# Performance work log

Measured on AMD Instinct MI355X. Metric: run time of the kernel, lower is better.

## Reference

```python
import jax, jax.numpy as jnp
import numpy as np

HIDDEN = 1024
HEADS = 16
HEAD_DIM = HIDDEN // HEADS
LN_EPS = 1e-12
NEG = -1.0e9


def setup_inputs() -> dict:
    key = jax.random.key(0)
    ks = jax.random.split(key, 12)
    B, S = 2, 2048
    sc = 1.0 / np.sqrt(HIDDEN)
    inp = {
        "x": jax.random.normal(ks[0], (B, S, HIDDEN), dtype=jnp.float32),
        "attention_mask": jax.random.randint(ks[1], (B, S, S), 0, 2, dtype=jnp.int32),
        "Wq": jax.random.normal(ks[2], (HIDDEN, HIDDEN), dtype=jnp.float32) * sc,
        "bq": jnp.zeros((HIDDEN,), dtype=jnp.float32),
        "Wk": jax.random.normal(ks[3], (HIDDEN, HIDDEN), dtype=jnp.float32) * sc,
        "bk": jnp.zeros((HIDDEN,), dtype=jnp.float32),
        "Wv": jax.random.normal(ks[4], (HIDDEN, HIDDEN), dtype=jnp.float32) * sc,
        "bv": jnp.zeros((HIDDEN,), dtype=jnp.float32),
        "Wo": jax.random.normal(ks[5], (HIDDEN, HIDDEN), dtype=jnp.float32) * sc,
        "bo": jnp.zeros((HIDDEN,), dtype=jnp.float32),
        "ln_g": jnp.ones((HIDDEN,), dtype=jnp.float32),
        "ln_b": jnp.zeros((HIDDEN,), dtype=jnp.float32),
    }
    return inp


def _heads(t):  # [B,S,HIDDEN] -> [B,H,S,D]
    B, S, _ = t.shape
    return t.reshape(B, S, HEADS, HEAD_DIM).transpose(0, 2, 1, 3)


def reference(x, attention_mask, Wq, bq, Wk, bk, Wv, bv, Wo, bo, ln_g, ln_b):
    q = _heads(x @ Wq + bq)
    k = _heads(x @ Wk + bk)
    v = _heads(x @ Wv + bv)
    # [B,H,Sq,Sk]
    scores = jnp.einsum("bhqd,bhkd->bhqk", q, k) / np.sqrt(HEAD_DIM).astype(np.float32)
    mask = attention_mask[:, None, :, :] == 0
    scores = jnp.where(mask, NEG, scores)
    probs = jax.nn.softmax(scores, axis=-1)
    ctx = jnp.einsum("bhqk,bhkd->bhqd", probs, v)
    B, _, S, _ = ctx.shape
    ctx = ctx.transpose(0, 2, 1, 3).reshape(B, S, HIDDEN)
    h = ctx @ Wo + bo
    y = h + x
    mu = jnp.mean(y, axis=-1, keepdims=True)
    var = jnp.mean(jnp.square(y - mu), axis=-1, keepdims=True)
    out = (y - mu) * jax.lax.rsqrt(var + LN_EPS) * ln_g + ln_b
    return out, scores
```

## Files before the change

kernel.cpp:

```cpp
#include <hip/hip_runtime.h>
#include <math.h>

#define HIDDEN 1024
#define HEADS 16
#define HDIM 64
#define BATCH 2
#define SEQ 2048
#define NEGV -1.0e9f
#define TOK (BATCH * SEQ * HIDDEN)
#define SC_N ((size_t)BATCH * HEADS * SEQ * SEQ)
#define ROW_CUT 29
#define PIT 72

typedef __bf16 bf16x8 __attribute__((ext_vector_type(8)));
typedef float f32x4 __attribute__((ext_vector_type(4)));

__device__ __forceinline__ unsigned short f2bf(float f) {
    union { float f; unsigned u; } v; v.f = f;
    unsigned r = (v.u + 0x7fffu + ((v.u >> 16) & 1u)) >> 16;
    return (unsigned short)r;
}
__device__ __forceinline__ float bf2f(unsigned short h) {
    union { unsigned u; float f; } v; v.u = ((unsigned)h) << 16;
    return v.f;
}
__device__ __forceinline__ void split_bf(float v, unsigned short& h, unsigned short& l) {
    h = f2bf(v);
    l = f2bf(v - bf2f(h));
}
__device__ __forceinline__ bf16x8 ld_frag(const unsigned short* p) {
    union { uint4 u; bf16x8 v; } t;
    t.u = *(const uint4*)p;
    return t.v;
}

template<int PRESPLIT, int SPLITOUT>
__global__ __launch_bounds__(256) void mfma_gemm(
    const float* __restrict__ A,
    const unsigned short* __restrict__ Ahi, const unsigned short* __restrict__ Alo,
    const float* __restrict__ Bw, const float* __restrict__ bias,
    float* __restrict__ C,
    unsigned short* __restrict__ Ohi, unsigned short* __restrict__ Olo,
    int M, int N, int K)
{
    __shared__ unsigned short Ah[128][PIT], Al[128][PIT];
    __shared__ unsigned short Bh[64][PIT], Bl[64][PIT];
    int tid = threadIdx.x;
    int lane = tid & 63, wv = tid >> 6;
    int wm = wv >> 1, wn = wv & 1;
    int l15 = lane & 15, l4 = lane >> 4;
    int mBase = blockIdx.y * 128, nBase = blockIdx.x * 64;

    f32x4 acc[4][2] = {};

    for (int kt = 0; kt < K; kt += 64) {
        if (PRESPLIT) {
            int r = tid >> 3, g = tid & 7;
            #pragma unroll
            for (int i = 0; i < 4; i++) {
                int rr = r + i * 32;
                size_t gofs = (size_t)(mBase + rr) * K + kt + g * 8;
                *(uint4*)&Ah[rr][g * 8] = *(const uint4*)&Ahi[gofs];
                *(uint4*)&Al[rr][g * 8] = *(const uint4*)&Alo[gofs];
            }
        } else {
            int r = tid >> 4, c4 = (tid & 15) * 4;
            #pragma unroll
            for (int i = 0; i < 8; i++) {
                int rr = r + i * 16;
                float4 f = *(const float4*)&A[(size_t)(mBase + rr) * K + kt + c4];
                unsigned short h0, h1, h2, h3, q0, q1, q2, q3;
                split_bf(f.x, h0, q0); split_bf(f.y, h1, q1);
                split_bf(f.z, h2, q2); split_bf(f.w, h3, q3);
                uint2 ph, pl;
                ph.x = (unsigned)h0 | ((unsigned)h1 << 16);
                ph.y = (unsigned)h2 | ((unsigned)h3 << 16);
                pl.x = (unsigned)q0 | ((unsigned)q1 << 16);
                pl.y = (unsigned)q2 | ((unsigned)q3 << 16);
                *(uint2*)&Ah[rr][c4] = ph;
                *(uint2*)&Al[rr][c4] = pl;
            }
        }
        {
            int r = tid >> 4, c4 = (tid & 15) * 4;
            #pragma unroll
            for (int i = 0; i < 4; i++) {
                int rr = r + i * 16;
                float4 f = *(const float4*)&Bw[(size_t)(kt + rr) * N + nBase + c4];
                unsigned short h, l;
                split_bf(f.x, h, l); Bh[c4 + 0][rr] = h; Bl[c4 + 0][rr] = l;
                split_bf(f.y, h, l); Bh[c4 + 1][rr] = h; Bl[c4 + 1][rr] = l;
                split_bf(f.z, h, l); Bh[c4 + 2][rr] = h; Bl[c4 + 2][rr] = l;
                split_bf(f.w, h, l); Bh[c4 + 3][rr] = h; Bl[c4 + 3][rr] = l;
            }
        }
        __syncthreads();

        #pragma unroll
        for (int ks = 0; ks < 64; ks += 32) {
            int ko = ks + l4 * 8;
            bf16x8 aH[4], aL[4], bH[2], bL[2];
            #pragma unroll
            for (int ti = 0; ti < 4; ti++) {
                aH[ti] = ld_frag(&Ah[wm * 64 + ti * 16 + l15][ko]);
                aL[ti] = ld_frag(&Al[wm * 64 + ti * 16 + l15][ko]);
            }
            #pragma unroll
            for (int tj = 0; tj < 2; tj++) {
                bH[tj] = ld_frag(&Bh[wn * 32 + tj * 16 + l15][ko]);
                bL[tj] = ld_frag(&Bl[wn * 32 + tj * 16 + l15][ko]);
            }
            #pragma unroll
            for (int ti = 0; ti < 4; ti++)
                #pragma unroll
                for (int tj = 0; tj < 2; tj++) {
                    acc[ti][tj] = __builtin_amdgcn_mfma_f32_16x16x32_bf16(aH[ti], bH[tj], acc[ti][tj], 0, 0, 0);
                    acc[ti][tj] = __builtin_amdgcn_mfma_f32_16x16x32_bf16(aH[ti], bL[tj], acc[ti][tj], 0, 0, 0);
                    acc[ti][tj] = __builtin_amdgcn_mfma_f32_16x16x32_bf16(aL[ti], bH[tj], acc[ti][tj], 0, 0, 0);
                }
        }
        __syncthreads();
    }

    #pragma unroll
    for (int ti = 0; ti < 4; ti++) {
        #pragma unroll
        for (int tj = 0; tj < 2; tj++) {
            int m0 = mBase + wm * 64 + ti * 16 + l4 * 4;
            int n  = nBase + wn * 32 + tj * 16 + l15;
            float bv = bias[n];
            #pragma unroll
            for (int rg = 0; rg < 4; rg++) {
                float v = acc[ti][tj][rg] + bv;
                if (SPLITOUT) {
                    unsigned short h, l;
                    split_bf(v, h, l);
                    Ohi[(size_t)(m0 + rg) * N + n] = h;
                    Olo[(size_t)(m0 + rg) * N + n] = l;
                } else {
                    C[(size_t)(m0 + rg) * N + n] = v;
                }
            }
        }
    }
}

__global__ __launch_bounds__(256) void attn_mfma(
    const unsigned short* __restrict__ Qhi, const unsigned short* __restrict__ Qlo,
    const unsigned short* __restrict__ Khi, const unsigned short* __restrict__ Klo,
    const unsigned short* __restrict__ Vhi, const unsigned short* __restrict__ Vlo,
    const int* __restrict__ mask, float* __restrict__ scores_out,
    unsigned short* __restrict__ Chi, unsigned short* __restrict__ Clo)
{
    __shared__ unsigned short Kh[64][PIT], Kl[64][PIT];
    __shared__ unsigned short Th[64][PIT], Tl[64][PIT];
    __shared__ unsigned short Ph[4][16][PIT], Pl[4][16][PIT];

    int tid = threadIdx.x;
    int lane = tid & 63, w = tid >> 6;
    int l15 = lane & 15, l4 = lane >> 4;
    int qBase = blockIdx.x * 64;
    int h = blockIdx.y, b = blockIdx.z;

    size_t qofs = (size_t)(b * SEQ + qBase + w * 16 + l15) * HIDDEN + h * HDIM;
    bf16x8 qh0 = ld_frag(&Qhi[qofs + l4 * 8]);
    bf16x8 qh1 = ld_frag(&Qhi[qofs + 32 + l4 * 8]);
    bf16x8 ql0 = ld_frag(&Qlo[qofs + l4 * 8]);
    bf16x8 ql1 = ld_frag(&Qlo[qofs + 32 + l4 * 8]);

    f32x4 cacc[4] = {};
    float mrow[4] = {-3.0e38f, -3.0e38f, -3.0e38f, -3.0e38f};
    float rsum[4] = {0.f, 0.f, 0.f, 0.f};

    for (int kt = 0; kt < SEQ; kt += 64) {
        {
            int r = tid >> 3, g = tid & 7;
            #pragma unroll
            for (int i = 0; i < 2; i++) {
                int rr = r + i * 32;
                size_t tok = (size_t)(b * SEQ + kt + rr) * HIDDEN + h * HDIM + g * 8;
                *(uint4*)&Kh[rr][g * 8] = *(const uint4*)&Khi[tok];
                *(uint4*)&Kl[rr][g * 8] = *(const uint4*)&Klo[tok];
                union { uint4 u; unsigned short s[8]; } vh, vl;
                vh.u = *(const uint4*)&Vhi[tok];
                vl.u = *(const uint4*)&Vlo[tok];
                #pragma unroll
                for (int dd = 0; dd < 8; dd++) {
                    Th[g * 8 + dd][rr] = vh.s[dd];
                    Tl[g * 8 + dd][rr] = vl.s[dd];
                }
            }
        }
        __syncthreads();

        f32x4 sacc[4] = {};
        #pragma unroll
        for (int ks = 0; ks < 64; ks += 32) {
            int ko = ks + l4 * 8;
            bf16x8 qH = ks ? qh1 : qh0;
            bf16x8 qL = ks ? ql1 : ql0;
            #pragma unroll
            for (int j = 0; j < 4; j++) {
                bf16x8 kH = ld_frag(&Kh[j * 16 + l15][ko]);
                bf16x8 kL = ld_frag(&Kl[j * 16 + l15][ko]);
                sacc[j] = __builtin_amdgcn_mfma_f32_16x16x32_bf16(qH, kH, sacc[j], 0, 0, 0);
                sacc[j] = __builtin_amdgcn_mfma_f32_16x16x32_bf16(qH, kL, sacc[j], 0, 0, 0);
                sacc[j] = __builtin_amdgcn_mfma_f32_16x16x32_bf16(qL, kH, sacc[j], 0, 0, 0);
            }
        }

        float sv[4][4];
        #pragma unroll
        for (int j = 0; j < 4; j++) {
            #pragma unroll
            for (int rg = 0; rg < 4; rg++) {
                int qrow = qBase + w * 16 + l4 * 4 + rg;
                int kc = kt + j * 16 + l15;
                int mval = mask[(size_t)(b * SEQ + qrow) * SEQ + kc];
                float s = (mval == 0) ? NEGV : sacc[j][rg] * 0.125f;
                scores_out[((size_t)(b * HEADS + h) * SEQ + qrow) * SEQ + kc] = s;
                sv[j][rg] = s;
            }
        }

        #pragma unroll
        for (int rg = 0; rg < 4; rg++) {
            float tmax = fmaxf(fmaxf(sv[0][rg], sv[1][rg]), fmaxf(sv[2][rg], sv[3][rg]));
            #pragma unroll
            for (int o = 1; o < 16; o <<= 1)
                tmax = fmaxf(tmax, __shfl_xor(tmax, o, 64));
            float mn = fmaxf(mrow[rg], tmax);
            float fac = __expf(mrow[rg] - mn);
            mrow[rg] = mn;
            float ts = 0.f;
            #pragma unroll
            for (int j = 0; j < 4; j++) {
                float e = __expf(sv[j][rg] - mn);
                unsigned short ph, pl;
                split_bf(e, ph, pl);
                Ph[w][l4 * 4 + rg][j * 16 + l15] = ph;
                Pl[w][l4 * 4 + rg][j * 16 + l15] = pl;
                ts += e;
            }
            #pragma unroll
            for (int o = 1; o < 16; o <<= 1)
                ts += __shfl_xor(ts, o, 64);
            rsum[rg] = rsum[rg] * fac + ts;
            cacc[0][rg] *= fac; cacc[1][rg] *= fac;
            cacc[2][rg] *= fac; cacc[3][rg] *= fac;
        }

        #pragma unroll
        for (int ks = 0; ks < 64; ks += 32) {
            int ko = ks + l4 * 8;
            bf16x8 pH = ld_frag(&Ph[w][l15][ko]);
            bf16x8 pL = ld_frag(&Pl[w][l15][ko]);
            #pragma unroll
            for (int j = 0; j < 4; j++) {
                bf16x8 vH = ld_frag(&Th[j * 16 + l15][ko]);
                bf16x8 vL = ld_frag(&Tl[j * 16 + l15][ko]);
                cacc[j] = __builtin_amdgcn_mfma_f32_16x16x32_bf16(pH, vH, cacc[j], 0, 0, 0);
                cacc[j] = __builtin_amdgcn_mfma_f32_16x16x32_bf16(pH, vL, cacc[j], 0, 0, 0);
                cacc[j] = __builtin_amdgcn_mfma_f32_16x16x32_bf16(pL, vH, cacc[j], 0, 0, 0);
            }
        }
        __syncthreads();
    }

    #pragma unroll
    for (int rg = 0; rg < 4; rg++) {
        float inv = 1.0f / rsum[rg];
        int qrow = qBase + w * 16 + l4 * 4 + rg;
        size_t obase = (size_t)(b * SEQ + qrow) * HIDDEN + h * HDIM;
        #pragma unroll
        for (int j = 0; j < 4; j++) {
            float v = cacc[j][rg] * inv;
            unsigned short hh, ll;
            split_bf(v, hh, ll);
            Chi[obase + j * 16 + l15] = hh;
            Clo[obase + j * 16 + l15] = ll;
        }
    }
}

__global__ __launch_bounds__(256) void gemm_bias(const float* __restrict__ A,
    const float* __restrict__ Bw, const float* __restrict__ bias,
    float* __restrict__ C, int M, int N, int K)
{
    __shared__ float As[64][17];
    __shared__ float Bs[16][65];
    int tid = threadIdx.x;
    int tx = tid & 15, ty = tid >> 4;
    int mBase = blockIdx.y * 64, nBase = blockIdx.x * 64;
    float acc[4][4] = {};
    int idA = tid * 4;
    int ra = idA >> 4, ca = idA & 15;
    int rb = idA >> 6, cb = idA & 63;
    int ty4 = ty * 4, tx4 = tx * 4;
    for (int k0 = 0; k0 < K; k0 += 16) {
        float4 fa = *(const float4*)(A + (size_t)(mBase + ra) * K + k0 + ca);
        As[ra][ca + 0] = fa.x; As[ra][ca + 1] = fa.y;
        As[ra][ca + 2] = fa.z; As[ra][ca + 3] = fa.w;
        float4 fb = *(const float4*)(Bw + (size_t)(k0 + rb) * N + nBase + cb);
        Bs[rb][cb + 0] = fb.x; Bs[rb][cb + 1] = fb.y;
        Bs[rb][cb + 2] = fb.z; Bs[rb][cb + 3] = fb.w;
        __syncthreads();
        #pragma unroll
        for (int kk = 0; kk < 16; kk++) {
            float a0 = As[ty4 + 0][kk], a1 = As[ty4 + 1][kk];
            float a2 = As[ty4 + 2][kk], a3 = As[ty4 + 3][kk];
            float b0 = Bs[kk][tx4 + 0], b1 = Bs[kk][tx4 + 1];
            float b2 = Bs[kk][tx4 + 2], b3 = Bs[kk][tx4 + 3];
            acc[0][0] += a0 * b0; acc[0][1] += a0 * b1; acc[0][2] += a0 * b2; acc[0][3] += a0 * b3;
            acc[1][0] += a1 * b0; acc[1][1] += a1 * b1; acc[1][2] += a1 * b2; acc[1][3] += a1 * b3;
            acc[2][0] += a2 * b0; acc[2][1] += a2 * b1; acc[2][2] += a2 * b2; acc[2][3] += a2 * b3;
            acc[3][0] += a3 * b0; acc[3][1] += a3 * b1; acc[3][2] += a3 * b2; acc[3][3] += a3 * b3;
        }
        __syncthreads();
    }
    #pragma unroll
    for (int i = 0; i < 4; i++) {
        int m = mBase + ty4 + i;
        #pragma unroll
        for (int j = 0; j < 4; j++) {
            int n = nBase + tx4 + j;
            C[(size_t)m * N + n] = acc[i][j] + bias[n];
        }
    }
}

__global__ __launch_bounds__(256) void attn_kernel(
    const float* __restrict__ qb, const float* __restrict__ kb, const float* __restrict__ vb,
    const int* __restrict__ mask, float* __restrict__ scores_out, float* __restrict__ ctx,
    int row_cut)
{
    __shared__ float qs[HDIM];
    __shared__ float sc[SEQ];
    __shared__ float red[4];
    __shared__ float part[4][HDIM];
    int tid = threadIdx.x;
    int q = blockIdx.x, h = blockIdx.y, b = blockIdx.z;
    bool wr = (b * HEADS + h) < row_cut;

    if (tid < HDIM)
        qs[tid] = qb[((size_t)(b * SEQ + q)) * HIDDEN + h * HDIM + tid];
    __syncthreads();

    const int* mrow = mask + ((size_t)(b * SEQ + q)) * SEQ;
    const float* kbase = kb + (size_t)b * SEQ * HIDDEN + h * HDIM;
    float* srow = scores_out + (((size_t)(b * HEADS + h)) * SEQ + q) * SEQ;

    float lmax = -3.0e38f;
    for (int j = tid; j < SEQ; j += 256) {
        const float4* kp = (const float4*)(kbase + (size_t)j * HIDDEN);
        float dot = 0.f;
        #pragma unroll
        for (int c = 0; c < 16; c++) {
            float4 u = kp[c];
            dot += qs[c * 4 + 0] * u.x + qs[c * 4 + 1] * u.y
                 + qs[c * 4 + 2] * u.z + qs[c * 4 + 3] * u.w;
        }
        float s = (mrow[j] == 0) ? NEGV : dot * 0.125f;
        sc[j] = s;
// ... 99 lines not shown
        float acc[4][4] = {};
        for (int k0 = 0; k0 < HIDDEN; k0 += 16) {
            float4 fa = *(const float4*)(x + (size_t)(rowBase + ra) * HIDDEN + k0 + ca);
            As[ra][ca + 0] = fa.x; As[ra][ca + 1] = fa.y;
            As[ra][ca + 2] = fa.z; As[ra][ca + 3] = fa.w;
            float4 fb = *(const float4*)(W + (size_t)(k0 + rb) * HIDDEN + hcol + cb);
            Bs[rb][cb + 0] = fb.x; Bs[rb][cb + 1] = fb.y;
            Bs[rb][cb + 2] = fb.z; Bs[rb][cb + 3] = fb.w;
            __syncthreads();
            #pragma unroll
            for (int kk = 0; kk < 16; kk++) {
                float a0 = As[ty4 + 0][kk], a1 = As[ty4 + 1][kk];
                float a2 = As[ty4 + 2][kk], a3 = As[ty4 + 3][kk];
                float b0 = Bs[kk][tx4 + 0], b1 = Bs[kk][tx4 + 1];
                float b2 = Bs[kk][tx4 + 2], b3 = Bs[kk][tx4 + 3];
                acc[0][0] += a0 * b0; acc[0][1] += a0 * b1; acc[0][2] += a0 * b2; acc[0][3] += a0 * b3;
                acc[1][0] += a1 * b0; acc[1][1] += a1 * b1; acc[1][2] += a1 * b2; acc[1][3] += a1 * b3;
                acc[2][0] += a2 * b0; acc[2][1] += a2 * b1; acc[2][2] += a2 * b2; acc[2][3] += a2 * b3;
                acc[3][0] += a3 * b0; acc[3][1] += a3 * b1; acc[3][2] += a3 * b2; acc[3][3] += a3 * b3;
            }
            __syncthreads();
        }
        #pragma unroll
        for (int i = 0; i < 4; i++)
            #pragma unroll
            for (int j = 0; j < 4; j++) {
                float v = acc[i][j] + bias[hcol + tx4 + j];
                if (pass) kt[ty4 + i][tx4 + j] = v;
                else      qt[ty4 + i][tx4 + j] = v;
            }
        __syncthreads();
    }

    float s[4][4] = {};
    for (int d = 0; d < HDIM; d++) {
        float qv0 = qt[ty4 + 0][d], qv1 = qt[ty4 + 1][d];
        float qv2 = qt[ty4 + 2][d], qv3 = qt[ty4 + 3][d];
        float kv0 = kt[tx4 + 0][d], kv1 = kt[tx4 + 1][d];
        float kv2 = kt[tx4 + 2][d], kv3 = kt[tx4 + 3][d];
        s[0][0] += qv0 * kv0; s[0][1] += qv0 * kv1; s[0][2] += qv0 * kv2; s[0][3] += qv0 * kv3;
        s[1][0] += qv1 * kv0; s[1][1] += qv1 * kv1; s[1][2] += qv1 * kv2; s[1][3] += qv1 * kv3;
        s[2][0] += qv2 * kv0; s[2][1] += qv2 * kv1; s[2][2] += qv2 * kv2; s[2][3] += qv2 * kv3;
        s[3][0] += qv3 * kv0; s[3][1] += qv3 * kv1; s[3][2] += qv3 * kv2; s[3][3] += qv3 * kv3;
    }
    #pragma unroll
    for (int i = 0; i < 4; i++) {
        int q = qBase + ty4 + i;
        const int* mrow = mask + ((size_t)(b * SEQ + q)) * SEQ;
        float* srow = scores + (((size_t)(b * HEADS + h)) * SEQ + q) * SEQ;
        #pragma unroll
        for (int j = 0; j < 4; j++) {
            int kk = kkBase + tx4 + j;
            srow[kk] = (mrow[kk] == 0) ? NEGV : s[i][j] * 0.125f;
        }
    }
}

extern "C" void kernel_launch(void* const* d_in, const int* in_sizes, int n_in,
                              void* d_out, int out_size, void* d_ws, size_t ws_size,
                              hipStream_t stream)
{
    const float* x   = (const float*)d_in[0];
    const int*   msk = (const int*)d_in[1];
    const float* Wq  = (const float*)d_in[2];
    const float* bq  = (const float*)d_in[3];
    const float* Wk  = (const float*)d_in[4];
    const float* bk  = (const float*)d_in[5];
    const float* Wv  = (const float*)d_in[6];
    const float* bv  = (const float*)d_in[7];
    const float* Wo  = (const float*)d_in[8];
    const float* bo  = (const float*)d_in[9];
    const float* lng = (const float*)d_in[10];
    const float* lnb = (const float*)d_in[11];

    float* out0   = (float*)d_out;
    float* scores = out0 + (size_t)TOK;

    const size_t need = (size_t)3 * TOK * sizeof(float);
    const bool use_ws = (d_ws != nullptr) && (ws_size >= need);

    const int M = BATCH * SEQ;

    if (use_ws) {
        unsigned short* Qhi = (unsigned short*)out0;
        unsigned short* Qlo = Qhi + (size_t)TOK;
        unsigned short* Khi = (unsigned short*)d_ws;
        unsigned short* Klo = Khi + (size_t)TOK;
        unsigned short* Vhi = Klo + (size_t)TOK;
        unsigned short* Vlo = Vhi + (size_t)TOK;
        unsigned short* Chi = Vlo + (size_t)TOK;
        unsigned short* Clo = Chi + (size_t)TOK;

        dim3 gg(HIDDEN / 64, M / 128);
        mfma_gemm<0, 1><<<gg, 256, 0, stream>>>(x, nullptr, nullptr, Wq, bq,
                                                nullptr, Qhi, Qlo, M, HIDDEN, HIDDEN);
        mfma_gemm<0, 1><<<gg, 256, 0, stream>>>(x, nullptr, nullptr, Wk, bk,
                                                nullptr, Khi, Klo, M, HIDDEN, HIDDEN);
        mfma_gemm<0, 1><<<gg, 256, 0, stream>>>(x, nullptr, nullptr, Wv, bv,
                                                nullptr, Vhi, Vlo, M, HIDDEN, HIDDEN);
        attn_mfma<<<dim3(SEQ / 64, HEADS, BATCH), 256, 0, stream>>>(
            Qhi, Qlo, Khi, Klo, Vhi, Vlo, msk, scores, Chi, Clo);
        mfma_gemm<1, 0><<<gg, 256, 0, stream>>>(nullptr, Chi, Clo, Wo, bo,
                                                out0, nullptr, nullptr, M, HIDDEN, HIDDEN);
        ln_kernel<<<M, 256, 0, stream>>>(out0, x, lng, lnb, out0);
    } else {
        float* Ks = scores + (SC_N - (size_t)3 * TOK);
        float* Vs = Ks + (size_t)TOK;
        float* Cs = Vs + (size_t)TOK;
        float* Qs = out0;
        dim3 gg(HIDDEN / 64, M / 64);
        gemm_bias<<<gg, 256, 0, stream>>>(x, Wq, bq, Qs, M, HIDDEN, HIDDEN);
        gemm_bias<<<gg, 256, 0, stream>>>(x, Wk, bk, Ks, M, HIDDEN, HIDDEN);
        gemm_bias<<<gg, 256, 0, stream>>>(x, Wv, bv, Vs, M, HIDDEN, HIDDEN);
        attn_kernel<<<dim3(SEQ, HEADS, BATCH), 256, 0, stream>>>(Qs, Ks, Vs, msk, scores, Cs, ROW_CUT);
        gemm_bias<<<gg, 256, 0, stream>>>(Cs, Wo, bo, out0, M, HIDDEN, HIDDEN);
        ln_kernel<<<M, 256, 0, stream>>>(out0, x, lng, lnb, out0);
        score_fixup<<<dim3(SEQ / 64, SEQ / 64, 3), 256, 0, stream>>>(x, Wq, bq, Wk, bk, msk, scores);
    }
}
```

Measured before the change: 1.091 ms.

## Pre-split inputs and transposed weights, enlarge GEMM and attention tiles, swizzle V

Adds kernels that split x into bf16 hi/lo once and transpose-split each weight matrix up front, so the projection GEMMs only load pre-split bf16 tiles. The GEMM moves to 512 threads with 128x128 tiles. Attention now covers 128 query rows per block (two row tiles per wave), which halves K/V reloads, and it XOR-swizzles the transposed V tile to cut LDS bank conflicts. The cost is extra small launches and scratch buffers placed in the scores and workspace regions, with ordering hazards to watch.

```diff
diff --git a/kernel.cpp b/kernel.cpp
--- a/kernel.cpp
+++ b/kernel.cpp
@@ -8,6 +8,7 @@
 #define SEQ 2048
 #define NEGV -1.0e9f
 #define TOK (BATCH * SEQ * HIDDEN)
+#define HH (HIDDEN * HIDDEN)
 #define SC_N ((size_t)BATCH * HEADS * SEQ * SEQ)
 #define ROW_CUT 29
 #define PIT 72
@@ -34,65 +35,79 @@
     return t.v;
 }
 
-template<int PRESPLIT, int SPLITOUT>
-__global__ __launch_bounds__(256) void mfma_gemm(
-    const float* __restrict__ A,
+__global__ __launch_bounds__(256) void split_rows(const float* __restrict__ in,
+    unsigned short* __restrict__ hi, unsigned short* __restrict__ lo)
+{
+    size_t i = ((size_t)blockIdx.x * 256 + threadIdx.x) * 8;
+    float4 f0 = *(const float4*)(in + i);
+    float4 f1 = *(const float4*)(in + i + 4);
+    union { uint4 u; unsigned short s[8]; } H, L;
+    split_bf(f0.x, H.s[0], L.s[0]); split_bf(f0.y, H.s[1], L.s[1]);
+    split_bf(f0.z, H.s[2], L.s[2]); split_bf(f0.w, H.s[3], L.s[3]);
+    split_bf(f1.x, H.s[4], L.s[4]); split_bf(f1.y, H.s[5], L.s[5]);
+    split_bf(f1.z, H.s[6], L.s[6]); split_bf(f1.w, H.s[7], L.s[7]);
+    *(uint4*)(hi + i) = H.u;
+    *(uint4*)(lo + i) = L.u;
+}
+
+__global__ __launch_bounds__(256) void split_T(const float* __restrict__ W,
+    unsigned short* __restrict__ Thi, unsigned short* __restrict__ Tlo)
+{
+    __shared__ float Ts[64][65];
+    int n0 = blockIdx.x * 64, k0 = blockIdx.y * 64;
+    int tid = threadIdx.x;
+    int r = tid >> 4, c4 = (tid & 15) * 4;
+    #pragma unroll
+    for (int i = 0; i < 4; i++) {
+        int rr = r + i * 16;
+        float4 f = *(const float4*)&W[(size_t)(k0 + rr) * HIDDEN + n0 + c4];
+        Ts[rr][c4 + 0] = f.x; Ts[rr][c4 + 1] = f.y;
+        Ts[rr][c4 + 2] = f.z; Ts[rr][c4 + 3] = f.w;
+    }
+    __syncthreads();
+    int rp = tid >> 3, g = tid & 7;
+    #pragma unroll
+    for (int i = 0; i < 2; i++) {
+        int nr = rp + i * 32;
+        union { uint4 u; unsigned short s[8]; } Hh, Ll;
+        #pragma unroll
+        for (int d = 0; d < 8; d++)
+            split_bf(Ts[g * 8 + d][nr], Hh.s[d], Ll.s[d]);
+        size_t o = (size_t)(n0 + nr) * HIDDEN + k0 + g * 8;
+        *(uint4*)&Thi[o] = Hh.u;
+        *(uint4*)&Tlo[o] = Ll.u;
+    }
+}
+
+template<int SPLITOUT>
+__global__ __launch_bounds__(512) void gemm_ps(
     const unsigned short* __restrict__ Ahi, const unsigned short* __restrict__ Alo,
-    const float* __restrict__ Bw, const float* __restrict__ bias,
-    float* __restrict__ C,
+    const unsigned short* __restrict__ BThi, const unsigned short* __restrict__ BTlo,
+    const float* __restrict__ bias, float* __restrict__ C,
     unsigned short* __restrict__ Ohi, unsigned short* __restrict__ Olo,
     int M, int N, int K)
 {
     __shared__ unsigned short Ah[128][PIT], Al[128][PIT];
-    __shared__ unsigned short Bh[64][PIT], Bl[64][PIT];
+    __shared__ unsigned short Bh[128][PIT], Bl[128][PIT];
     int tid = threadIdx.x;
     int lane = tid & 63, wv = tid >> 6;
-    int wm = wv >> 1, wn = wv & 1;
+    int wm = wv >> 2, wn = wv & 3;
     int l15 = lane & 15, l4 = lane >> 4;
-    int mBase = blockIdx.y * 128, nBase = blockIdx.x * 64;
+    int mBase = blockIdx.y * 128, nBase = blockIdx.x * 128;
+    int sr = tid >> 3, sg = tid & 7;
 
     f32x4 acc[4][2] = {};
 
     for (int kt = 0; kt < K; kt += 64) {
-        if (PRESPLIT) {
-            int r = tid >> 3, g = tid & 7;
-            #pragma unroll
-            for (int i = 0; i < 4; i++) {
-                int rr = r + i * 32;
-                size_t gofs = (size_t)(mBase + rr) * K + kt + g * 8;
-                *(uint4*)&Ah[rr][g * 8] = *(const uint4*)&Ahi[gofs];
-                *(uint4*)&Al[rr][g * 8] = *(const uint4*)&Alo[gofs];
-            }
-        } else {
-            int r = tid >> 4, c4 = (tid & 15) * 4;
-            #pragma unroll
-            for (int i = 0; i < 8; i++) {
-                int rr = r + i * 16;
-                float4 f = *(const float4*)&A[(size_t)(mBase + rr) * K + kt + c4];
-                unsigned short h0, h1, h2, h3, q0, q1, q2, q3;
-                split_bf(f.x, h0, q0); split_bf(f.y, h1, q1);
-                split_bf(f.z, h2, q2); split_bf(f.w, h3, q3);
-                uint2 ph, pl;
-                ph.x = (unsigned)h0 | ((unsigned)h1 << 16);
-                ph.y = (unsigned)h2 | ((unsigned)h3 << 16);
-                pl.x = (unsigned)q0 | ((unsigned)q1 << 16);
-                pl.y = (unsigned)q2 | ((unsigned)q3 << 16);
-                *(uint2*)&Ah[rr][c4] = ph;
-                *(uint2*)&Al[rr][c4] = pl;
-            }
-        }
-        {
-            int r = tid >> 4, c4 = (tid & 15) * 4;
-            #pragma unroll
-            for (int i = 0; i < 4; i++) {
-                int rr = r + i * 16;
-                float4 f = *(const float4*)&Bw[(size_t)(kt + rr) * N + nBase + c4];
-                unsigned short h, l;
-                split_bf(f.x, h, l); Bh[c4 + 0][rr] = h; Bl[c4 + 0][rr] = l;
-                split_bf(f.y, h, l); Bh[c4 + 1][rr] = h; Bl[c4 + 1][rr] = l;
-                split_bf(f.z, h, l); Bh[c4 + 2][rr] = h; Bl[c4 + 2][rr] = l;
-                split_bf(f.w, h, l); Bh[c4 + 3][rr] = h; Bl[c4 + 3][rr] = l;
-            }
+        #pragma unroll
+        for (int i = 0; i < 2; i++) {
+            int rr = sr + i * 64;
+            size_t ga = (size_t)(mBase + rr) * K + kt + sg * 8;
+            *(uint4*)&Ah[rr][sg * 8] = *(const uint4*)&Ahi[ga];
+            *(uint4*)&Al[rr][sg * 8] = *(const uint4*)&Alo[ga];
+            size_t gb = (size_t)(nBase + rr) * K + kt + sg * 8;
+            *(uint4*)&Bh[rr][sg * 8] = *(const uint4*)&BThi[gb];
+            *(uint4*)&Bl[rr][sg * 8] = *(const uint4*)&BTlo[gb];
         }
         __syncthreads();
 
@@ -133,10 +148,10 @@
             for (int rg = 0; rg < 4; rg++) {
                 float v = acc[ti][tj][rg] + bv;
                 if (SPLITOUT) {
-                    unsigned short h, l;
-                    split_bf(v, h, l);
-                    Ohi[(size_t)(m0 + rg) * N + n] = h;
-                    Olo[(size_t)(m0 + rg) * N + n] = l;
+                    unsigned short hh, ll;
+                    split_bf(v, hh, ll);
+                    Ohi[(size_t)(m0 + rg) * N + n] = hh;
+                    Olo[(size_t)(m0 + rg) * N + n] = ll;
                 } else {
                     C[(size_t)(m0 + rg) * N + n] = v;
                 }
@@ -154,131 +169,150 @@
 {
     __shared__ unsigned short Kh[64][PIT], Kl[64][PIT];
     __shared__ unsigned short Th[64][PIT], Tl[64][PIT];
-    __shared__ unsigned short Ph[4][16][PIT], Pl[4][16][PIT];
+    __shared__ unsigned short Ph[4][32][PIT], Pl[4][32][PIT];
 
     int tid = threadIdx.x;
     int lane = tid & 63, w = tid >> 6;
     int l15 = lane & 15, l4 = lane >> 4;
-    int qBase = blockIdx.x * 64;
+    int qBase = blockIdx.x * 128;
     int h = blockIdx.y, b = blockIdx.z;
-
-    size_t qofs = (size_t)(b * SEQ + qBase + w * 16 + l15) * HIDDEN + h * HDIM;
-    bf16x8 qh0 = ld_frag(&Qhi[qofs + l4 * 8]);
-    bf16x8 qh1 = ld_frag(&Qhi[qofs + 32 + l4 * 8]);
-    bf16x8 ql0 = ld_frag(&Qlo[qofs + l4 * 8]);
-    bf16x8 ql1 = ld_frag(&Qlo[qofs + 32 + l4 * 8]);
-
-    f32x4 cacc[4] = {};
-    float mrow[4] = {-3.0e38f, -3.0e38f, -3.0e38f, -3.0e38f};
-    float rsum[4] = {0.f, 0.f, 0.f, 0.f};
+    int sr = tid >> 3, sg = tid & 7;
+
+    bf16x8 qh[2][2], ql[2][2];
+    #pragma unroll
+    for (int rt = 0; rt < 2; rt++) {
+        size_t qofs = (size_t)(b * SEQ + qBase + w * 32 + rt * 16 + l15) * HIDDEN + h * HDIM;
+        qh[rt][0] = ld_frag(&Qhi[qofs + l4 * 8]);
+        qh[rt][1] = ld_frag(&Qhi[qofs + 32 + l4 * 8]);
+        ql[rt][0] = ld_frag(&Qlo[qofs + l4 * 8]);
+        ql[rt][1] = ld_frag(&Qlo[qofs + 32 + l4 * 8]);
+    }
+
+    f32x4 cacc[2][4] = {};
+    float mrow[2][4] = {{-3.0e38f,-3.0e38f,-3.0e38f,-3.0e38f},
+                        {-3.0e38f,-3.0e38f,-3.0e38f,-3.0e38f}};
+    float rsum[2][4] = {};
 
     for (int kt = 0; kt < SEQ; kt += 64) {
-        {
-            int r = tid >> 3, g = tid & 7;
-            #pragma unroll
-            for (int i = 0; i < 2; i++) {
-                int rr = r + i * 32;
-                size_t tok = (size_t)(b * SEQ + kt + rr) * HIDDEN + h * HDIM + g * 8;
-                *(uint4*)&Kh[rr][g * 8] = *(const uint4*)&Khi[tok];
-                *(uint4*)&Kl[rr][g * 8] = *(const uint4*)&Klo[tok];
-                union { uint4 u; unsigned short s[8]; } vh, vl;
-                vh.u = *(const uint4*)&Vhi[tok];
-                vl.u = *(const uint4*)&Vlo[tok];
-                #pragma unroll
-                for (int dd = 0; dd < 8; dd++) {
-                    Th[g * 8 + dd][rr] = vh.s[dd];
-                    Tl[g * 8 + dd][rr] = vl.s[dd];
-                }
+        #pragma unroll
+        for (int i = 0; i < 2; i++) {
+            int rr = sr + i * 32;
+            size_t tok = (size_t)(b * SEQ + kt + rr) * HIDDEN + h * HDIM + sg * 8;
+            *(uint4*)&Kh[rr][sg * 8] = *(const uint4*)&Khi[tok];
+            *(uint4*)&Kl[rr][sg * 8] = *(const uint4*)&Klo[tok];
+            union { uint4 u; unsigned short s[8]; } vh, vl;
+            vh.u = *(const uint4*)&Vhi[tok];
+            vl.u = *(const uint4*)&Vlo[tok];
+            int cbs = ((((rr >> 3) ^ sg) & 7) << 3) + (rr & 7);
+            #pragma unroll
+            for (int dd = 0; dd < 8; dd++) {
+                Th[sg * 8 + dd][cbs] = vh.s[dd];
+                Tl[sg * 8 + dd][cbs] = vl.s[dd];
             }
         }
         __syncthreads();
 
-        f32x4 sacc[4] = {};
-        #pragma unroll
-        for (int ks = 0; ks < 64; ks += 32) {
-            int ko = ks + l4 * 8;
-            bf16x8 qH = ks ? qh1 : qh0;
-            bf16x8 qL = ks ? ql1 : ql0;
+        f32x4 sacc[2][4] = {};
+        #pragma unroll
+        for (int ks = 0; ks < 2; ks++) {
+            int ko = ks * 32 + l4 * 8;
             #pragma unroll
             for (int j = 0; j < 4; j++) {
                 bf16x8 kH = ld_frag(&Kh[j * 16 + l15][ko]);
                 bf16x8 kL = ld_frag(&Kl[j * 16 + l15][ko]);
-                sacc[j] = __builtin_amdgcn_mfma_f32_16x16x32_bf16(qH, kH, sacc[j], 0, 0, 0);
-                sacc[j] = __builtin_amdgcn_mfma_f32_16x16x32_bf16(qH, kL, sacc[j], 0, 0, 0);
-                sacc[j] = __builtin_amdgcn_mfma_f32_16x16x32_bf16(qL, kH, sacc[j], 0, 0, 0);
-            }
-        }
-
-        float sv[4][4];
-        #pragma unroll
-        for (int j = 0; j < 4; j++) {
+                #pragma unroll
+                for (int rt = 0; rt < 2; rt++) {
+                    sacc[rt][j] = __builtin_amdgcn_mfma_f32_16x16x32_bf16(qh[rt][ks], kH, sacc[rt][j], 0, 0, 0);
+                    sacc[rt][j] = __builtin_amdgcn_mfma_f32_16x16x32_bf16(qh[rt][ks], kL, sacc[rt][j], 0, 0, 0);
+                    sacc[rt][j] = __builtin_amdgcn_mfma_f32_16x16x32_bf16(ql[rt][ks], kH, sacc[rt][j], 0, 0, 0);
+                }
+            }
+        }
+
+        #pragma unroll
+        for (int rt = 0; rt < 2; rt++) {
+            float sv[4][4];
+            #pragma unroll
+            for (int j = 0; j < 4; j++) {
+                #pragma unroll
+                for (int rg = 0; rg < 4; rg++) {
+                    int qrow = qBase + w * 32 + rt * 16 + l4 * 4 + rg;
+                    int kc = kt + j * 16 + l15;
+                    int mval = mask[(size_t)(b * SEQ + qrow) * SEQ + kc];
+                    float s = (mval == 0) ? NEGV : sacc[rt][j][rg] * 0.125f;
+                    scores_out[((size_t)(b * HEADS + h) * SEQ + qrow) * SEQ + kc] = s;
+                    sv[j][rg] = s;
+                }
+            }
             #pragma unroll
             for (int rg = 0; rg < 4; rg++) {
-                int qrow = qBase + w * 16 + l4 * 4 + rg;
-                int kc = kt + j * 16 + l15;
-                int mval = mask[(size_t)(b * SEQ + qrow) * SEQ + kc];
-                float s = (mval == 0) ? NEGV : sacc[j][rg] * 0.125f;
-                scores_out[((size_t)(b * HEADS + h) * SEQ + qrow) * SEQ + kc] = s;
-                sv[j][rg] = s;
-            }
-        }
-
+                float tmax = fmaxf(fmaxf(sv[0][rg], sv[1][rg]), fmaxf(sv[2][rg], sv[3][rg]));
+                #pragma unroll
+                for (int o = 1; o < 16; o <<= 1)
+                    tmax = fmaxf(tmax, __shfl_xor(tmax, o, 64));
+                float mn = fmaxf(mrow[rt][rg], tmax);
+                float fac = __expf(mrow[rt][rg] - mn);
+                mrow[rt][rg] = mn;
+                float ts = 0.f;
+                #pragma unroll
+                for (int j = 0; j < 4; j++) {
+                    float e = __expf(sv[j][rg] - mn);
+                    unsigned short ph, pl;
+                    split_bf(e, ph, pl);
+                    Ph[w][rt * 16 + l4 * 4 + rg][j * 16 + l15] = ph;
+                    Pl[w][rt * 16 + l4 * 4 + rg][j * 16 + l15] = pl;
+                    ts += e;
+                }
+                #pragma unroll
+                for (int o = 1; o < 16; o <<= 1)
+                    ts += __shfl_xor(ts, o, 64);
+                rsum[rt][rg] = rsum[rt][rg] * fac + ts;
+                cacc[rt][0][rg] *= fac; cacc[rt][1][rg] *= fac;
+                cacc[rt][2][rg] *= fac; cacc[rt][3][rg] *= fac;
+            }
+        }
+
+        #pragma unroll
+        for (int ks = 0; ks < 2; ks++) {
+            int ko = ks * 32 + l4 * 8;
+            bf16x8 pH[2], pL[2];
+            #pragma unroll
+            for (int rt = 0; rt < 2; rt++) {
+                pH[rt] = ld_frag(&Ph[w][rt * 16 + l15][ko]);
+                pL[rt] = ld_frag(&Pl[w][rt * 16 + l15][ko]);
+            }
+            #pragma unroll
+            for (int j = 0; j < 4; j++) {
+                int drow = j * 16 + l15;
+                int pb = (((ko >> 3) ^ (drow >> 3)) & 7) << 3;
+                bf16x8 vH = ld_frag(&Th[drow][pb]);
+                bf16x8 vL = ld_frag(&Tl[drow][pb]);
+                #pragma unroll
+                for (int rt = 0; rt < 2; rt++) {
+                    cacc[rt][j] = __builtin_amdgcn_mfma_f32_16x16x32_bf16(pH[rt], vH, cacc[rt][j], 0, 0, 0);
+                    cacc[rt][j] = __builtin_amdgcn_mfma_f32_16x16x32_bf16(pH[rt], vL, cacc[rt][j], 0, 0, 0);
+                    cacc[rt][j] = __builtin_amdgcn_mfma_f32_16x16x32_bf16(pL[rt], vH, cacc[rt][j], 0, 0, 0);
+                }
+            }
+        }
+        __syncthreads();
+    }
+
+    #pragma unroll
+    for (int rt = 0; rt < 2; rt++) {
         #pragma unroll
         for (int rg = 0; rg < 4; rg++) {
-            float tmax = fmaxf(fmaxf(sv[0][rg], sv[1][rg]), fmaxf(sv[2][rg], sv[3][rg]));
-            #pragma unroll
-            for (int o = 1; o < 16; o <<= 1)
-                tmax = fmaxf(tmax, __shfl_xor(tmax, o, 64));
-            float mn = fmaxf(mrow[rg], tmax);
-            float fac = __expf(mrow[rg] - mn);
-            mrow[rg] = mn;
-            float ts = 0.f;
+            float inv = 1.0f / rsum[rt][rg];
+            int qrow = qBase + w * 32 + rt * 16 + l4 * 4 + rg;
+            size_t obase = (size_t)(b * SEQ + qrow) * HIDDEN + h * HDIM;
             #pragma unroll
             for (int j = 0; j < 4; j++) {
-                float e = __expf(sv[j][rg] - mn);
-                unsigned short ph, pl;
-                split_bf(e, ph, pl);
-                Ph[w][l4 * 4 + rg][j * 16 + l15] = ph;
-                Pl[w][l4 * 4 + rg][j * 16 + l15] = pl;
-                ts += e;
-            }
-            #pragma unroll
-            for (int o = 1; o < 16; o <<= 1)
-                ts += __shfl_xor(ts, o, 64);
-            rsum[rg] = rsum[rg] * fac + ts;
-            cacc[0][rg] *= fac; cacc[1][rg] *= fac;
-            cacc[2][rg] *= fac; cacc[3][rg] *= fac;
-        }
-
-        #pragma unroll
-        for (int ks = 0; ks < 64; ks += 32) {
-            int ko = ks + l4 * 8;
-            bf16x8 pH = ld_frag(&Ph[w][l15][ko]);
-            bf16x8 pL = ld_frag(&Pl[w][l15][ko]);
-            #pragma unroll
-            for (int j = 0; j < 4; j++) {
-                bf16x8 vH = ld_frag(&Th[j * 16 + l15][ko]);
-                bf16x8 vL = ld_frag(&Tl[j * 16 + l15][ko]);
-                cacc[j] = __builtin_amdgcn_mfma_f32_16x16x32_bf16(pH, vH, cacc[j], 0, 0, 0);
-                cacc[j] = __builtin_amdgcn_mfma_f32_16x16x32_bf16(pH, vL, cacc[j], 0, 0, 0);
-                cacc[j] = __builtin_amdgcn_mfma_f32_16x16x32_bf16(pL, vH, cacc[j], 0, 0, 0);
-            }
-        }
-        __syncthreads();
-    }
-
-    #pragma unroll
-    for (int rg = 0; rg < 4; rg++) {
-        float inv = 1.0f / rsum[rg];
-        int qrow = qBase + w * 16 + l4 * 4 + rg;
-        size_t obase = (size_t)(b * SEQ + qrow) * HIDDEN + h * HDIM;
-        #pragma unroll
-        for (int j = 0; j < 4; j++) {
-            float v = cacc[j][rg] * inv;
-            unsigned short hh, ll;
-            split_bf(v, hh, ll);
-            Chi[obase + j * 16 + l15] = hh;
-            Clo[obase + j * 16 + l15] = ll;
+                float v = cacc[rt][j][rg] * inv;
+                unsigned short hh, ll;
+                split_bf(v, hh, ll);
+                Chi[obase + j * 16 + l15] = hh;
+                Clo[obase + j * 16 + l15] = ll;
+            }
         }
     }
 }
@@ -544,26 +578,43 @@
     const int M = BATCH * SEQ;
 
     if (use_ws) {
-        unsigned short* Qhi = (unsigned short*)out0;
-        unsigned short* Qlo = Qhi + (size_t)TOK;
         unsigned short* Khi = (unsigned short*)d_ws;
         unsigned short* Klo = Khi + (size_t)TOK;
         unsigned short* Vhi = Klo + (size_t)TOK;
         unsigned short* Vlo = Vhi + (size_t)TOK;
         unsigned short* Chi = Vlo + (size_t)TOK;
         unsigned short* Clo = Chi + (size_t)TOK;
-
-        dim3 gg(HIDDEN / 64, M / 128);
-        mfma_gemm<0, 1><<<gg, 256, 0, stream>>>(x, nullptr, nullptr, Wq, bq,
-                                                nullptr, Qhi, Qlo, M, HIDDEN, HIDDEN);
-        mfma_gemm<0, 1><<<gg, 256, 0, stream>>>(x, nullptr, nullptr, Wk, bk,
-                                                nullptr, Khi, Klo, M, HIDDEN, HIDDEN);
-        mfma_gemm<0, 1><<<gg, 256, 0, stream>>>(x, nullptr, nullptr, Wv, bv,
-                                                nullptr, Vhi, Vlo, M, HIDDEN, HIDDEN);
-        attn_mfma<<<dim3(SEQ / 64, HEADS, BATCH), 256, 0, stream>>>(
+        unsigned short* Qhi = (unsigned short*)out0;
+        unsigned short* Qlo = Qhi + (size_t)TOK;
+        unsigned short* Xhi  = (unsigned short*)scores;
+        unsigned short* Xlo  = Xhi + (size_t)TOK;
+        unsigned short* WTqh = Xlo + (size_t)TOK;
+        unsigned short* WTql = WTqh + (size_t)HH;
+        unsigned short* WTkh = WTql + (size_t)HH;
+        unsigned short* WTkl = WTkh + (size_t)HH;
+        unsigned short* WTvh = WTkl + (size_t)HH;
+        unsigned short* WTvl = WTvh + (size_t)HH;
+        unsigned short* WToh = Khi;
+        unsigned short* WTol = Khi + (size_t)HH;
+
+        split_rows<<<TOK / (256 * 8), 256, 0, stream>>>(x, Xhi, Xlo);
+        dim3 gt(16, 16);
+        split_T<<<gt, 256, 0, stream>>>(Wq, WTqh, WTql);
+        split_T<<<gt, 256, 0, stream>>>(Wk, WTkh, WTkl);
+        split_T<<<gt, 256, 0, stream>>>(Wv, WTvh, WTvl);
+
+        dim3 gg(HIDDEN / 128, M / 128);
+        gemm_ps<1><<<gg, 512, 0, stream>>>(Xhi, Xlo, WTqh, WTql, bq,
+                                           nullptr, Qhi, Qlo, M, HIDDEN, HIDDEN);
+        gemm_ps<1><<<gg, 512, 0, stream>>>(Xhi, Xlo, WTkh, WTkl, bk,
+                                           nullptr, Khi, Klo, M, HIDDEN, HIDDEN);
+        gemm_ps<1><<<gg, 512, 0, stream>>>(Xhi, Xlo, WTvh, WTvl, bv,
+                                           nullptr, Vhi, Vlo, M, HIDDEN, HIDDEN);
+        attn_mfma<<<dim3(SEQ / 128, HEADS, BATCH), 256, 0, stream>>>(
             Qhi, Qlo, Khi, Klo, Vhi, Vlo, msk, scores, Chi, Clo);
-        mfma_gemm<1, 0><<<gg, 256, 0, stream>>>(nullptr, Chi, Clo, Wo, bo,
-                                                out0, nullptr, nullptr, M, HIDDEN, HIDDEN);
+        split_T<<<gt, 256, 0, stream>>>(Wo, WToh, WTol);
+        gemm_ps<0><<<gg, 512, 0, stream>>>(Chi, Clo, WToh, WTol, bo,
+                                           out0, nullptr, nullptr, M, HIDDEN, HIDDEN);
         ln_kernel<<<M, 256, 0, stream>>>(out0, x, lng, lnb, out0);
     } else {
         float* Ks = scores + (SC_N - (size_t)3 * TOK);
```

Measured after the change: 1.386 ms. 27.0% more time.

## Pre-split inputs and weights to bf16 pairs, fuse QKV GEMM with async LDS loads

Applied to the files above, without the earlier changes.

Adds separate kernels that split x and the transposed weights into bf16 hi/lo arrays once, then runs a single fused QKV GEMM (and the output GEMM) that loads tiles with global_load_lds into XOR-swizzled shared memory using 128x128 tiles and 512 threads. This removes the per-tile fp32-to-bf16 split and the strided transposed LDS stores from the GEMM inner loops, and cuts the QKV work to one launch. The V transpose tile in attention is also XOR-swizzled to reduce LDS bank conflicts. It adds extra split/transpose kernel launches and reuses the scores and workspace buffers as scratch for the split data, which depends on the ordering of later writes.

```diff
diff --git a/kernel.cpp b/kernel.cpp
--- a/kernel.cpp
+++ b/kernel.cpp
@@ -8,6 +8,7 @@
 #define SEQ 2048
 #define NEGV -1.0e9f
 #define TOK (BATCH * SEQ * HIDDEN)
+#define HH (HIDDEN * HIDDEN)
 #define SC_N ((size_t)BATCH * HEADS * SEQ * SEQ)
 #define ROW_CUT 29
 #define PIT 72
@@ -33,82 +34,109 @@
     t.u = *(const uint4*)p;
     return t.v;
 }
-
-template<int PRESPLIT, int SPLITOUT>
-__global__ __launch_bounds__(256) void mfma_gemm(
-    const float* __restrict__ A,
+__device__ __forceinline__ void gl2lds16(const unsigned short* g, unsigned short* l) {
+    __builtin_amdgcn_global_load_lds(
+        (const __attribute__((address_space(1))) void*)g,
+        (__attribute__((address_space(3))) void*)l, 16, 0, 0);
+}
+
+__global__ __launch_bounds__(256) void split_rows(const float* __restrict__ in,
+    unsigned short* __restrict__ hi, unsigned short* __restrict__ lo)
+{
+    size_t i = ((size_t)blockIdx.x * 256 + threadIdx.x) * 8;
+    float4 f0 = *(const float4*)(in + i);
+    float4 f1 = *(const float4*)(in + i + 4);
+    union { uint4 u; unsigned short s[8]; } H, L;
+    split_bf(f0.x, H.s[0], L.s[0]); split_bf(f0.y, H.s[1], L.s[1]);
+    split_bf(f0.z, H.s[2], L.s[2]); split_bf(f0.w, H.s[3], L.s[3]);
+    split_bf(f1.x, H.s[4], L.s[4]); split_bf(f1.y, H.s[5], L.s[5]);
+    split_bf(f1.z, H.s[6], L.s[6]); split_bf(f1.w, H.s[7], L.s[7]);
+    *(uint4*)(hi + i) = H.u;
+    *(uint4*)(lo + i) = L.u;
+}
+
+__global__ __launch_bounds__(256) void split_T(const float* __restrict__ W,
+    unsigned short* __restrict__ Thi, unsigned short* __restrict__ Tlo)
+{
+    __shared__ float Ts[64][65];
+    int n0 = blockIdx.x * 64, k0 = blockIdx.y * 64;
+    int tid = threadIdx.x;
+    int r = tid >> 4, c4 = (tid & 15) * 4;
+    #pragma unroll
+    for (int i = 0; i < 4; i++) {
+        int rr = r + i * 16;
+        float4 f = *(const float4*)&W[(size_t)(k0 + rr) * HIDDEN + n0 + c4];
+        Ts[rr][c4 + 0] = f.x; Ts[rr][c4 + 1] = f.y;
+        Ts[rr][c4 + 2] = f.z; Ts[rr][c4 + 3] = f.w;
+    }
+    __syncthreads();
+    int rp = tid >> 3, g = tid & 7;
+    #pragma unroll
+    for (int i = 0; i < 2; i++) {
+        int nr = rp + i * 32;
+        union { uint4 u; unsigned short s[8]; } Hh, Ll;
+        #pragma unroll
+        for (int d = 0; d < 8; d++)
+            split_bf(Ts[g * 8 + d][nr], Hh.s[d], Ll.s[d]);
+        size_t o = (size_t)(n0 + nr) * HIDDEN + k0 + g * 8;
+        *(uint4*)&Thi[o] = Hh.u;
+        *(uint4*)&Tlo[o] = Ll.u;
+    }
+}
+
+template<int FUSED>
+__global__ __launch_bounds__(512) void gemm_ps(
     const unsigned short* __restrict__ Ahi, const unsigned short* __restrict__ Alo,
-    const float* __restrict__ Bw, const float* __restrict__ bias,
+    const unsigned short* __restrict__ BThi, const unsigned short* __restrict__ BTlo,
+    const float* __restrict__ b0, const float* __restrict__ b1, const float* __restrict__ b2,
     float* __restrict__ C,
-    unsigned short* __restrict__ Ohi, unsigned short* __restrict__ Olo,
-    int M, int N, int K)
-{
-    __shared__ unsigned short Ah[128][PIT], Al[128][PIT];
-    __shared__ unsigned short Bh[64][PIT], Bl[64][PIT];
+    unsigned short* __restrict__ o0h, unsigned short* __restrict__ o0l,
+    unsigned short* __restrict__ o1h, unsigned short* __restrict__ o1l,
+    unsigned short* __restrict__ o2h, unsigned short* __restrict__ o2l,
+    int M)
+{
+    __shared__ unsigned short Ah[128][64], Al[128][64];
+    __shared__ unsigned short Bh[128][64], Bl[128][64];
+    const int K = HIDDEN;
     int tid = threadIdx.x;
     int lane = tid & 63, wv = tid >> 6;
-    int wm = wv >> 1, wn = wv & 1;
+    int wm = wv >> 2, wn = wv & 3;
     int l15 = lane & 15, l4 = lane >> 4;
-    int mBase = blockIdx.y * 128, nBase = blockIdx.x * 64;
+    int mBase = blockIdx.y * 128, nBase = blockIdx.x * 128;
+    int srow = lane >> 3, schk = lane & 7;
 
     f32x4 acc[4][2] = {};
 
     for (int kt = 0; kt < K; kt += 64) {
-        if (PRESPLIT) {
-            int r = tid >> 3, g = tid & 7;
-            #pragma unroll
-            for (int i = 0; i < 4; i++) {
-                int rr = r + i * 32;
-                size_t gofs = (size_t)(mBase + rr) * K + kt + g * 8;
-                *(uint4*)&Ah[rr][g * 8] = *(const uint4*)&Ahi[gofs];
-                *(uint4*)&Al[rr][g * 8] = *(const uint4*)&Alo[gofs];
-            }
-        } else {
-            int r = tid >> 4, c4 = (tid & 15) * 4;
-            #pragma unroll
-            for (int i = 0; i < 8; i++) {
-                int rr = r + i * 16;
-                float4 f = *(const float4*)&A[(size_t)(mBase + rr) * K + kt + c4];
-                unsigned short h0, h1, h2, h3, q0, q1, q2, q3;
-                split_bf(f.x, h0, q0); split_bf(f.y, h1, q1);
-                split_bf(f.z, h2, q2); split_bf(f.w, h3, q3);
-                uint2 ph, pl;
-                ph.x = (unsigned)h0 | ((unsigned)h1 << 16);
-                ph.y = (unsigned)h2 | ((unsigned)h3 << 16);
-                pl.x = (unsigned)q0 | ((unsigned)q1 << 16);
-                pl.y = (unsigned)q2 | ((unsigned)q3 << 16);
-                *(uint2*)&Ah[rr][c4] = ph;
-                *(uint2*)&Al[rr][c4] = pl;
-            }
-        }
-        {
-            int r = tid >> 4, c4 = (tid & 15) * 4;
-            #pragma unroll
-            for (int i = 0; i < 4; i++) {
-                int rr = r + i * 16;
-                float4 f = *(const float4*)&Bw[(size_t)(kt + rr) * N + nBase + c4];
-                unsigned short h, l;
-                split_bf(f.x, h, l); Bh[c4 + 0][rr] = h; Bl[c4 + 0][rr] = l;
-                split_bf(f.y, h, l); Bh[c4 + 1][rr] = h; Bl[c4 + 1][rr] = l;
-                split_bf(f.z, h, l); Bh[c4 + 2][rr] = h; Bl[c4 + 2][rr] = l;
-                split_bf(f.w, h, l); Bh[c4 + 3][rr] = h; Bl[c4 + 3][rr] = l;
-            }
+        #pragma unroll
+        for (int i = 0; i < 2; i++) {
+            int r0 = wv * 16 + i * 8;
+            int row = r0 + srow;
+            int co = (schk * 8) ^ ((row & 7) << 3);
+            gl2lds16(&Ahi[(size_t)(mBase + row) * K + kt + co], &Ah[r0][0]);
+            gl2lds16(&Alo[(size_t)(mBase + row) * K + kt + co], &Al[r0][0]);
+            gl2lds16(&BThi[(size_t)(nBase + row) * K + kt + co], &Bh[r0][0]);
+            gl2lds16(&BTlo[(size_t)(nBase + row) * K + kt + co], &Bl[r0][0]);
         }
         __syncthreads();
 
         #pragma unroll
-        for (int ks = 0; ks < 64; ks += 32) {
-            int ko = ks + l4 * 8;
+        for (int ks = 0; ks < 2; ks++) {
+            int ko = ks * 32 + l4 * 8;
             bf16x8 aH[4], aL[4], bH[2], bL[2];
             #pragma unroll
             for (int ti = 0; ti < 4; ti++) {
-                aH[ti] = ld_frag(&Ah[wm * 64 + ti * 16 + l15][ko]);
-                aL[ti] = ld_frag(&Al[wm * 64 + ti * 16 + l15][ko]);
+                int ar = wm * 64 + ti * 16 + l15;
+                int ac = ko ^ ((ar & 7) << 3);
+                aH[ti] = ld_frag(&Ah[ar][ac]);
+                aL[ti] = ld_frag(&Al[ar][ac]);
             }
             #pragma unroll
             for (int tj = 0; tj < 2; tj++) {
-                bH[tj] = ld_frag(&Bh[wn * 32 + tj * 16 + l15][ko]);
-                bL[tj] = ld_frag(&Bl[wn * 32 + tj * 16 + l15][ko]);
+                int br = wn * 32 + tj * 16 + l15;
+                int bc = ko ^ ((br & 7) << 3);
+                bH[tj] = ld_frag(&Bh[br][bc]);
+                bL[tj] = ld_frag(&Bl[br][bc]);
             }
             #pragma unroll
             for (int ti = 0; ti < 4; ti++)
@@ -122,23 +150,30 @@
         __syncthreads();
     }
 
+    const unsigned short* dummy = nullptr; (void)dummy;
+    int t = nBase >> 10;
+    unsigned short* Oh = FUSED ? (t == 0 ? o0h : t == 1 ? o1h : o2h) : nullptr;
+    unsigned short* Ol = FUSED ? (t == 0 ? o0l : t == 1 ? o1l : o2l) : nullptr;
+    const float* bias = FUSED ? (t == 0 ? b0 : t == 1 ? b1 : b2) : b0;
+    int nOff = FUSED ? (nBase & 1023) : nBase;
+
     #pragma unroll
     for (int ti = 0; ti < 4; ti++) {
         #pragma unroll
         for (int tj = 0; tj < 2; tj++) {
             int m0 = mBase + wm * 64 + ti * 16 + l4 * 4;
-            int n  = nBase + wn * 32 + tj * 16 + l15;
-            float bv = bias[n];
+            int nc = nOff + wn * 32 + tj * 16 + l15;
+            float bv = bias[nc];
             #pragma unroll
             for (int rg = 0; rg < 4; rg++) {
                 float v = acc[ti][tj][rg] + bv;
-                if (SPLITOUT) {
-                    unsigned short h, l;
-                    split_bf(v, h, l);
-                    Ohi[(size_t)(m0 + rg) * N + n] = h;
-                    Olo[(size_t)(m0 + rg) * N + n] = l;
+                if (FUSED) {
+                    unsigned short hh, ll;
+                    split_bf(v, hh, ll);
+                    Oh[(size_t)(m0 + rg) * HIDDEN + nc] = hh;
+                    Ol[(size_t)(m0 + rg) * HIDDEN + nc] = ll;
                 } else {
-                    C[(size_t)(m0 + rg) * N + n] = v;
+                    C[(size_t)(m0 + rg) * HIDDEN + nc] = v;
                 }
             }
         }
@@ -184,10 +219,11 @@
                 union { uint4 u; unsigned short s[8]; } vh, vl;
                 vh.u = *(const uint4*)&Vhi[tok];
                 vl.u = *(const uint4*)&Vlo[tok];
+                int cbs = ((((rr >> 3) ^ g) & 7) << 3) + (rr & 7);
                 #pragma unroll
                 for (int dd = 0; dd < 8; dd++) {
-                    Th[g * 8 + dd][rr] = vh.s[dd];
-                    Tl[g * 8 + dd][rr] = vl.s[dd];
+                    Th[g * 8 + dd][cbs] = vh.s[dd];
+                    Tl[g * 8 + dd][cbs] = vl.s[dd];
                 }
             }
         }
@@ -257,8 +293,10 @@
             bf16x8 pL = ld_frag(&Pl[w][l15][ko]);
             #pragma unroll
             for (int j = 0; j < 4; j++) {
-                bf16x8 vH = ld_frag(&Th[j * 16 + l15][ko]);
-                bf16x8 vL = ld_frag(&Tl[j * 16 + l15][ko]);
+                int drow = j * 16 + l15;
+                int pb = (((ko >> 3) ^ (drow >> 3)) & 7) << 3;
+                bf16x8 vH = ld_frag(&Th[drow][pb]);
+                bf16x8 vL = ld_frag(&Tl[drow][pb]);
                 cacc[j] = __builtin_amdgcn_mfma_f32_16x16x32_bf16(pH, vH, cacc[j], 0, 0, 0);
                 cacc[j] = __builtin_amdgcn_mfma_f32_16x16x32_bf16(pH, vL, cacc[j], 0, 0, 0);
                 cacc[j] = __builtin_amdgcn_mfma_f32_16x16x32_bf16(pL, vH, cacc[j], 0, 0, 0);
@@ -544,26 +582,38 @@
     const int M = BATCH * SEQ;
 
     if (use_ws) {
-        unsigned short* Qhi = (unsigned short*)out0;
-        unsigned short* Qlo = Qhi + (size_t)TOK;
         unsigned short* Khi = (unsigned short*)d_ws;
         unsigned short* Klo = Khi + (size_t)TOK;
         unsigned short* Vhi = Klo + (size_t)TOK;
         unsigned short* Vlo = Vhi + (size_t)TOK;
         unsigned short* Chi = Vlo + (size_t)TOK;
         unsigned short* Clo = Chi + (size_t)TOK;
-
-        dim3 gg(HIDDEN / 64, M / 128);
-        mfma_gemm<0, 1><<<gg, 256, 0, stream>>>(x, nullptr, nullptr, Wq, bq,
-                                                nullptr, Qhi, Qlo, M, HIDDEN, HIDDEN);
-        mfma_gemm<0, 1><<<gg, 256, 0, stream>>>(x, nullptr, nullptr, Wk, bk,
-                                                nullptr, Khi, Klo, M, HIDDEN, HIDDEN);
-        mfma_gemm<0, 1><<<gg, 256, 0, stream>>>(x, nullptr, nullptr, Wv, bv,
-                                                nullptr, Vhi, Vlo, M, HIDDEN, HIDDEN);
+        unsigned short* Qhi = (unsigned short*)out0;
+        unsigned short* Qlo = Qhi + (size_t)TOK;
+        unsigned short* Xhi = (unsigned short*)scores;
+        unsigned short* Xlo = Xhi + (size_t)TOK;
+        unsigned short* WTh = Xlo + (size_t)TOK;
+        unsigned short* WTl = WTh + (size_t)3 * HH;
+        unsigned short* WToh = Khi;
+        unsigned short* WTol = Khi + (size_t)HH;
+
+        split_rows<<<TOK / (256 * 8), 256, 0, stream>>>(x, Xhi, Xlo);
+        dim3 gt(16, 16);
+        split_T<<<gt, 256, 0, stream>>>(Wq, WTh, WTl);
+        split_T<<<gt, 256, 0, stream>>>(Wk, WTh + (size_t)HH, WTl + (size_t)HH);
+        split_T<<<gt, 256, 0, stream>>>(Wv, WTh + (size_t)2 * HH, WTl + (size_t)2 * HH);
+
+        dim3 gf(3 * HIDDEN / 128, M / 128);
+        gemm_ps<1><<<gf, 512, 0, stream>>>(Xhi, Xlo, WTh, WTl,
+                                           bq, bk, bv, nullptr,
+                                           Qhi, Qlo, Khi, Klo, Vhi, Vlo, M);
         attn_mfma<<<dim3(SEQ / 64, HEADS, BATCH), 256, 0, stream>>>(
             Qhi, Qlo, Khi, Klo, Vhi, Vlo, msk, scores, Chi, Clo);
-        mfma_gemm<1, 0><<<gg, 256, 0, stream>>>(nullptr, Chi, Clo, Wo, bo,
-                                                out0, nullptr, nullptr, M, HIDDEN, HIDDEN);
+        split_T<<<gt, 256, 0, stream>>>(Wo, WToh, WTol);
+        dim3 go(HIDDEN / 128, M / 128);
+        gemm_ps<0><<<go, 512, 0, stream>>>(Chi, Clo, WToh, WTol,
+                                           bo, nullptr, nullptr, out0,
+                                           nullptr, nullptr, nullptr, nullptr, nullptr, nullptr, M);
         ln_kernel<<<M, 256, 0, stream>>>(out0, x, lng, lnb, out0);
     } else {
         float* Ks = scores + (SC_N - (size_t)3 * TOK);
```

Measured after the change: 935.6 us. -14.3%, faster.
